# Kernel optimization log

Hardware: AMD Instinct MI355X
Metric: run time of the kernel (lower is better)

Reference implementation:

```python
import math
import jax
import jax.numpy as jnp
from jax import lax
import numpy as np

B, T, S, C, E = 16, 1024, 2048, 256, 256
STRIDE, MAX_SAMPLES, SIGMA, RAND_START = 20, 20, 3.0, 0


def setup_inputs():
    key = jax.random.key(0)
    ks = jax.random.split(key, 6)
    return {
        "x": jax.random.normal(ks[0], (B, T, C), jnp.float32),
        "target_embedding": jax.random.normal(ks[1], (B, T, E), jnp.float32),
        # scale keys so pre-softmax scores are O(1..10) like a trained model
        "enc_keys": jax.random.normal(ks[2], (B, E, S), jnp.float32) * 0.05,
        "enc_values": jax.random.normal(ks[3], (B, S, E), jnp.float32),
        "W_in": jax.random.normal(ks[4], (E, C), jnp.float32) * math.sqrt(1.0 / C),
        "b_in": jnp.zeros((E,), jnp.float32),
        "W_out": jax.random.normal(ks[5], (C, E), jnp.float32) * math.sqrt(1.0 / E),
        "b_out": jnp.zeros((C,), jnp.float32),
    }


def _get_matrix(attn, sim_vec, stride, start):
    # attn: [B,T,S], sim_vec: [B,S,E]
    nrm = sim_vec / jnp.linalg.norm(sim_vec, axis=2, keepdims=True)
    attn_avg = jnp.mean(attn, axis=1)[..., None]          # [B,S,1]
    ns = nrm[:, start::stride, :]                          # [B,N,E]
    aa = attn_avg[:, start::stride, :]                     # [B,N,1]
    sim = jnp.einsum('bne,bme->bnm', ns, ns)               # cosine similarity
    qual = aa @ jnp.swapaxes(aa, 1, 2)                     # quality outer product
    return qual * sim                                      # DPP kernel L [B,N,N]


def _bfgm(L, max_samples):
    # Vectorized faithful version of the greedy Cholesky DPP MAP loop.
    Bv, N, _ = L.shape
    bidx = jnp.arange(Bv)
    D0 = jnp.diagonal(L, axis1=1, axis2=2)                 # [B,N]
    mask0 = jnp.ones((Bv, N), L.dtype)
    J0 = jnp.argmax(jnp.log(D0 * mask0), axis=1)
    mask0 = mask0.at[bidx, J0].set(0.0)
    C0 = jnp.zeros((Bv, N, max_samples), L.dtype)          # col 0 stays zero (as in torch)

    def step(carry, t):
        Cm, D, J, mask = carry
        Lj = L[bidx, J, :]                                 # [B,N] = L[b, J[b], i]
        cj = Cm[bidx, J, :]                                # [B,K]
        cdot = jnp.einsum('bnk,bk->bn', Cm, cj)            # <c_i, c_j>
        dj = D[bidx, J][:, None]
        e = (Lj - cdot) / dj * mask                        # zero at already-selected
        Cm = Cm.at[:, :, t].set(e)
        D = D - e * e
        J = jnp.argmax(jnp.log(D * mask), axis=1)
        mask = mask.at[bidx, J].set(0.0)
        return (Cm, D, J, mask), J

    (_, _, _, _), Js = lax.scan(step, (C0, D0, J0, mask0), jnp.arange(1, max_samples))
    all_J = jnp.concatenate([J0[None, :], Js], axis=0).T   # [B,max_samples]
    return jnp.sort(all_J, axis=1)                         # = nonzero(1-mask) order


def _create_gm(mu, sigma, length):
    pos = jnp.arange(length, dtype=jnp.float32)            # [S]
    z = pos[None, None, :] - mu[:, :, None].astype(jnp.float32)
    g = jnp.exp(-(z * z) / (2.0 * sigma * sigma)) / (math.sqrt(2.0 * math.pi) * sigma)
    return jnp.sum(g, axis=1)                              # [B,S]


def _forward(x, target_embedding, enc_keys, enc_values, W_in, b_in, W_out, b_out):
    residual = x
    h = (jnp.einsum('btc,ec->bte', x, W_in) + b_in + target_embedding) * math.sqrt(0.5)
    scores = jnp.einsum('bte,bes->bts', h, enc_keys)       # [B,T,S]
    attn = jax.nn.softmax(scores, axis=-1)
    # DPP auxiliary KL loss (training path, encoder_padding_mask=None); the
    # kernel / greedy selection / target distribution carry no gradient.
    L = _get_matrix(lax.stop_gradient(attn), lax.stop_gradient(enc_values), STRIDE, RAND_START)
    mu = _bfgm(L, MAX_SAMPLES)
    dist = jax.nn.softmax(_create_gm(mu, SIGMA, scores.shape[2]), axis=1)
    x_mean = jnp.mean(attn, axis=1)                        # [B,S]
    kl = jnp.sum(x_mean * (jnp.log(x_mean) - dist))        # KLDivLoss(input=dist, target=x_mean, sum)
    out = jnp.einsum('bts,bse->bte', attn, enc_values)
    s = enc_values.shape[1]
    out = out * (s * math.sqrt(1.0 / s))                   # = sqrt(s)
    out = (jnp.einsum('bte,ce->btc', out, W_out) + b_out + residual) * math.sqrt(0.5)
    return out, attn, -kl


def reference(x, target_embedding, enc_keys, enc_values, W_in, b_in, W_out, b_out):
    return _forward(x, target_embedding, enc_keys, enc_values, W_in, b_in, W_out, b_out)
```

## Files before the change

### kernel.cpp

```cpp
#include <hip/hip_runtime.h>
#include <math.h>

#define BB 16
#define TT 1024
#define SS 2048
#define CC 256
#define EE 256
#define NSUB 103
#define MAXS 20
#define STRIDE_ 20
#define XCH 32

static constexpr float RSQRT2  = 0.70710678118654752440f;
static constexpr float SQRT_S  = 45.25483399593904f;
static constexpr float GNORM   = 0.13298076013381093f;
static constexpr float INV2S2  = 0.055555555555555555f;

typedef __attribute__((ext_vector_type(8))) __bf16 bf16x8;
typedef __attribute__((ext_vector_type(4))) float  f32x4;

__device__ __forceinline__ float wave_sum(float v) {
    #pragma unroll
    for (int o = 32; o; o >>= 1) v += __shfl_down(v, o);
    return v;
}
__device__ __forceinline__ float wave_max(float v) {
    #pragma unroll
    for (int o = 32; o; o >>= 1) v = fmaxf(v, __shfl_down(v, o));
    return v;
}
__device__ __forceinline__ unsigned short f2bf(float f) {
    unsigned int u = __float_as_uint(f);
    u = (u + 0x7FFFu + ((u >> 16) & 1u)) >> 16;
    return (unsigned short)u;
}
__device__ __forceinline__ float bf2f(unsigned short s) {
    return __uint_as_float(((unsigned int)s) << 16);
}

#define GLD_LDS16(g, l) __builtin_amdgcn_global_load_lds(                      \
    (const __attribute__((address_space(1))) void*)(g),                        \
    (__attribute__((address_space(3))) void*)(l), 16, 0, 0)

__global__ __launch_bounds__(256) void k_cast3(
    const float* __restrict__ a,  unsigned short* __restrict__ oa, int na,
    const float* __restrict__ b2, unsigned short* __restrict__ ob, int nb,
    const float* __restrict__ c2, unsigned short* __restrict__ oc, int nc)
{
    int i = blockIdx.x * 256 + threadIdx.x;
    const float* in; unsigned short* out;
    if (i < na)                { in = a;  out = oa; }
    else if (i < na + nb)      { in = b2; out = ob; i -= na; }
    else if (i < na + nb + nc) { in = c2; out = oc; i -= na + nb; }
    else return;
    const float4 v = reinterpret_cast<const float4*>(in)[i];
    union { unsigned short u[4]; unsigned long long v8; } pk;
    pk.u[0] = f2bf(v.x); pk.u[1] = f2bf(v.y);
    pk.u[2] = f2bf(v.z); pk.u[3] = f2bf(v.w);
    reinterpret_cast<unsigned long long*>(out)[i] = pk.v8;
}

__global__ __launch_bounds__(256) void k_transpose2(
    const float* __restrict__ keys, unsigned short* __restrict__ keysT,
    const float* __restrict__ vals, unsigned short* __restrict__ valsT)
{
    __shared__ float t[64][65];
    const int id = blockIdx.x;
    const float* in; unsigned short* out;
    int R, Cc, bx, by, b;
    if (id < 2048) {
        in = keys; out = keysT; R = EE; Cc = SS;
        bx = id & 3; by = (id >> 2) & 31; b = id >> 7;
    } else {
        const int id2 = id - 2048;
        in = vals; out = valsT; R = SS; Cc = EE;
        bx = id2 & 31; by = (id2 >> 5) & 3; b = id2 >> 7;
    }
    const int r0 = bx * 64, c0 = by * 64;
    const float* ip = in + (size_t)b * R * Cc;
    unsigned short* op = out + (size_t)b * R * Cc;
    const int tx = threadIdx.x & 63, ty = threadIdx.x >> 6;
    #pragma unroll
    for (int i = 0; i < 16; ++i)
        t[ty + 4 * i][tx] = ip[(size_t)(r0 + ty + 4 * i) * Cc + c0 + tx];
    __syncthreads();
    #pragma unroll
    for (int i = 0; i < 16; ++i)
        op[(size_t)(c0 + ty + 4 * i) * R + r0 + tx] = f2bf(t[tx][ty + 4 * i]);
}

template<int BM, int BN, int MODE>
__global__ __launch_bounds__(256) void k_gemm(
    const unsigned short* __restrict__ Abase,
    const unsigned short* __restrict__ Btbase,
    const float* __restrict__ bias, const float* __restrict__ add,
    float* __restrict__ Obase, unsigned short* __restrict__ Obbase,
    int M, int Nn, int K, float scale)
{
    constexpr int BK = 64;
    constexpr int AR = BM / 32;
    constexpr int BR = BN / 32;
    constexpr int WM = BM / 2, WN = BN / 2;
    constexpr int MI = WM / 16, NJ = WN / 16;

    __shared__ unsigned short As[BM * BK];
    __shared__ unsigned short Bs[BN * BK];

    const int nwg = gridDim.x * gridDim.y * gridDim.z;
    int l = blockIdx.x + gridDim.x * (blockIdx.y + gridDim.y * blockIdx.z);
    if ((nwg & 7) == 0) l = (l & 7) * (nwg >> 3) + (l >> 3);
    const int bx = l % gridDim.x; l /= gridDim.x;
    const int by = l % gridDim.y;
    const int b  = l / gridDim.y;

    const int m0 = bx * BM;
    const int n0 = by * BN;
    const unsigned short* A  = Abase  + (size_t)b * M  * K;
    const unsigned short* Bt = Btbase + (size_t)b * Nn * K;

    const int tid  = threadIdx.x;
    const int w    = tid >> 6;
    const int lane = tid & 63;
    const int wm   = w & 1, wn = w >> 1;

    const int sr  = tid >> 3;
    const int skb = ((tid & 7) << 4) ^ ((sr & 7) << 4);
    const unsigned short* ga[AR];
    const unsigned short* gb[BR];
    #pragma unroll
    for (int p = 0; p < AR; ++p)
        ga[p] = A + (size_t)(m0 + p * 32 + sr) * K + (skb >> 1);
    #pragma unroll
    for (int p = 0; p < BR; ++p)
        gb[p] = Bt + (size_t)(n0 + p * 32 + sr) * K + (skb >> 1);

    const int fr = lane & 15;
    const int qb = (lane >> 4) << 4;

    f32x4 acc[MI][NJ];
    #pragma unroll
    for (int i = 0; i < MI; ++i)
        #pragma unroll
        for (int j = 0; j < NJ; ++j)
            acc[i][j] = (f32x4){0.f, 0.f, 0.f, 0.f};

    for (int k0 = 0; k0 < K; k0 += BK) {
        #pragma unroll
        for (int p = 0; p < AR; ++p) GLD_LDS16(ga[p], As + p * 2048 + w * 512);
        #pragma unroll
        for (int p = 0; p < BR; ++p) GLD_LDS16(gb[p], Bs + p * 2048 + w * 512);
        #pragma unroll
        for (int p = 0; p < AR; ++p) ga[p] += BK;
        #pragma unroll
        for (int p = 0; p < BR; ++p) gb[p] += BK;
        __syncthreads();
        #pragma unroll
        for (int c = 0; c < 2; ++c) {
            bf16x8 af[MI], bf[NJ];
            #pragma unroll
            for (int i = 0; i < MI; ++i) {
                const int row = wm * WM + i * 16 + fr;
                const int byt = row * 128 + ((c * 64 + qb) ^ ((row & 7) << 4));
                af[i] = *reinterpret_cast<const bf16x8*>(
                            reinterpret_cast<const char*>(As) + byt);
            }
            #pragma unroll
            for (int j = 0; j < NJ; ++j) {
                const int row = wn * WN + j * 16 + fr;
                const int byt = row * 128 + ((c * 64 + qb) ^ ((row & 7) << 4));
                bf[j] = *reinterpret_cast<const bf16x8*>(
                            reinterpret_cast<const char*>(Bs) + byt);
            }
            #pragma unroll
            for (int i = 0; i < MI; ++i)
                #pragma unroll
                for (int j = 0; j < NJ; ++j)
                    acc[i][j] = __builtin_amdgcn_mfma_f32_16x16x32_bf16(af[i], bf[j], acc[i][j], 0, 0, 0);
        }
        __syncthreads();
    }

    float* Of = (MODE == 0 || MODE == 1) ? Obase + (size_t)b * M * Nn : nullptr;
    unsigned short* Ob = (MODE == 2 || MODE == 3) ? Obbase + (size_t)b * M * Nn : nullptr;
    const int rb = (lane >> 4) * 4;
    #pragma unroll
    for (int i = 0; i < MI; ++i)
        #pragma unroll
        for (int j = 0; j < NJ; ++j) {
            const int n = n0 + wn * WN + j * 16 + fr;
            #pragma unroll
            for (int r2 = 0; r2 < 4; ++r2) {
                const int m = m0 + wm * WM + i * 16 + rb + r2;
                const size_t idx = (size_t)m * Nn + n;
                if (MODE == 0) {
                    Of[idx] = acc[i][j][r2] * scale;
                } else if (MODE == 1) {
                    Of[idx] = (acc[i][j][r2] + bias[n] + add[idx]) * RSQRT2;
                } else if (MODE == 2) {
                    Ob[idx] = f2bf((acc[i][j][r2] + bias[n] + add[idx]) * RSQRT2);
                } else {
                    Ob[idx] = f2bf(acc[i][j][r2] * scale);
                }
            }
        }
}

__global__ __launch_bounds__(256) void k_softmax(float* __restrict__ attn,
                                                 unsigned short* __restrict__ attnb)
{
    const int row  = blockIdx.x * 4 + (threadIdx.x >> 6);
    const int lane = threadIdx.x & 63;
    float* p = attn + (size_t)row * SS;
    unsigned short* pb = attnb + (size_t)row * SS;

    float v[32];
    #pragma unroll
    for (int s = 0; s < 4; ++s) {
        union { unsigned short u[8]; uint4 q; } ld;
        ld.q = *reinterpret_cast<const uint4*>(&pb[s * 512 + lane * 8]);
        #pragma unroll
        for (int i = 0; i < 8; ++i) v[s * 8 + i] = bf2f(ld.u[i]);
    }
    float mx = v[0];
    #pragma unroll
    for (int i = 1; i < 32; ++i) mx = fmaxf(mx, v[i]);
    #pragma unroll
    for (int o = 32; o; o >>= 1) mx = fmaxf(mx, __shfl_xor(mx, o));
    float s = 0.f;
    #pragma unroll
    for (int i = 0; i < 32; ++i) { v[i] = expf(v[i] - mx); s += v[i]; }
    #pragma unroll
    for (int o = 32; o; o >>= 1) s += __shfl_xor(s, o);
    const float inv = 1.0f / s;
    #pragma unroll
    for (int seg = 0; seg < 4; ++seg) {
        float4 o0, o1;
        o0.x = v[seg * 8 + 0] * inv; o0.y = v[seg * 8 + 1] * inv;
        o0.z = v[seg * 8 + 2] * inv; o0.w = v[seg * 8 + 3] * inv;
        o1.x = v[seg * 8 + 4] * inv; o1.y = v[seg * 8 + 5] * inv;
        o1.z = v[seg * 8 + 6] * inv; o1.w = v[seg * 8 + 7] * inv;
        *reinterpret_cast<float4*>(&p[seg * 512 + lane * 8])     = o0;
        *reinterpret_cast<float4*>(&p[seg * 512 + lane * 8 + 4]) = o1;
        union { unsigned short u[8]; uint4 q; } pk;
        pk.u[0] = f2bf(o0.x); pk.u[1] = f2bf(o0.y); pk.u[2] = f2bf(o0.z); pk.u[3] = f2bf(o0.w);
        pk.u[4] = f2bf(o1.x); pk.u[5] = f2bf(o1.y); pk.u[6] = f2bf(o1.z); pk.u[7] = f2bf(o1.w);
        *reinterpret_cast<uint4*>(&pb[seg * 512 + lane * 8]) = pk.q;
    }
}

__global__ __launch_bounds__(256) void k_xmean_part(const unsigned short* __restrict__ attnb,
                                                    float* __restrict__ part,
                                                    float* __restrict__ klp)
{
    const int c = blockIdx.x, b = blockIdx.y;
    if (c == 0 && b == 0 && threadIdx.x == 0) klp[0] = 0.0f;
    const unsigned short* p = attnb + ((size_t)b * TT + (size_t)c * (TT / XCH)) * SS
                              + threadIdx.x * 8;
    float acc[8] = {0.f, 0.f, 0.f, 0.f, 0.f, 0.f, 0.f, 0.f};
    #pragma unroll 8
    for (int t = 0; t < TT / XCH; ++t) {
        union { unsigned short u[8]; uint4 v4; } ld;
        ld.v4 = *reinterpret_cast<const uint4*>(p + (size_t)t * SS);
        #pragma unroll
        for (int i = 0; i < 8; ++i) acc[i] += bf2f(ld.u[i]);
    }
    float* o = part + ((size_t)b * XCH + c) * SS + threadIdx.x * 8;
    #pragma unroll
    for (int i = 0; i < 8; ++i) o[i] = acc[i];
}

__global__ __launch_bounds__(128) void k_L_direct(const float* __restrict__ ev,
                                                  const float* __restrict__ part,
                                                  float* __restrict__ Lm)
{
    const int i = blockIdx.x, b = blockIdx.y;
    const int tid = threadIdx.x;
    __shared__ float evi[EE];
    __shared__ float aaS[NSUB];
    __shared__ float w[2];
    const float* rowi = ev + ((size_t)b * SS + (size_t)i * STRIDE_) * EE;
    const float v0 = rowi[tid], v1 = rowi[tid + 128];
    evi[tid] = v0; evi[tid + 128] = v1;
    const float r = wave_sum(v0 * v0 + v1 * v1);
    if ((tid & 63) == 0) w[tid >> 6] = r;
    if (tid < NSUB) {
        float s = 0.f;
        #pragma unroll 8
        for (int c2 = 0; c2 < XCH; ++c2)
            s += part[((size_t)b * XCH + c2) * SS + tid * STRIDE_];
        aaS[tid] = s * (1.0f / TT);
    }
    __syncthreads();
    const float nrmi = sqrtf(w[0] + w[1]);
    const float ai = aaS[i];
    for (int j = tid; j < NSUB; j += 128) {
        const float* rj = ev + ((size_t)b * SS + (size_t)j * STRIDE_) * EE;
        float d = 0.f, n2 = 0.f;
        #pragma unroll 4
        for (int e = 0; e < EE; e += 4) {
            const float4 a4 = *reinterpret_cast<const float4*>(&evi[e]);
            const float4 b4 = *reinterpret_cast<const float4*>(&rj[e]);
            d  += a4.x * b4.x + a4.y * b4.y + a4.z * b4.z + a4.w * b4.w;
            n2 += b4.x * b4.x + b4.y * b4.y + b4.z * b4.z + b4.w * b4.w;
        }
        Lm[((size_t)b * NSUB + i) * NSUB + j] = d * ai * aaS[j] / (nrmi * sqrtf(n2));
    }
}

__global__ __launch_bounds__(256) void k_bfgm_kl(const float* __restrict__ Lm,
                                                 const float* __restrict__ part,
                                                 float* __restrict__ outkl)
{
    const int b = blockIdx.x;
    const int tid = threadIdx.x;
    const float* L = Lm + (size_t)b * NSUB * NSUB;
    __shared__ float CmL[128 * 21];
    __shared__ float musS[MAXS];
    __shared__ float w[4];

    float xm[8];
    #pragma unroll
    for (int i = 0; i < 8; ++i) {
        float s = 0.f;
        #pragma unroll 8
        for (int c2 = 0; c2 < XCH; ++c2)
            s += part[((size_t)b * XCH + c2) * SS + tid + (i << 8)];
        xm[i] = s * (1.0f / TT);
    }

    if (tid < 64) {
        const int i0 = tid, i1 = tid + 64;
        const bool a1 = (i1 < NSUB);
        float D0 = L[(size_t)i0 * NSUB + i0];
        float D1 = a1 ? L[(size_t)i1 * NSUB + i1] : 0.0f;
        float m0 = 1.0f, m1 = a1 ? 1.0f : 0.0f;
        #pragma unroll
        for (int k = 0; k < MAXS; ++k) { CmL[i0 * 21 + k] = 0.0f; CmL[i1 * 21 + k] = 0.0f; }
        #pragma unroll 1
        for (int t = 0; t < MAXS; ++t) {
            float k0 = logf(D0 * m0); if (isnan(k0)) k0 = INFINITY;
            float k1 = a1 ? logf(D1 * m1) : -INFINITY; if (isnan(k1)) k1 = INFINITY;
            float v = k0; int idx = i0;
            if (k1 > v) { v = k1; idx = i1; }
            #pragma unroll
            for (int o = 32; o; o >>= 1) {
                const float ov = __shfl_down(v, o);
                const int   oi = __shfl_down(idx, o);
                if (ov > v || (ov == v && oi < idx)) { v = ov; idx = oi; }
            }
            const int J = __shfl(idx, 0);
            if (J == i0) m0 = 0.0f;
            if (J == i1) m1 = 0.0f;
            if (tid == 0) musS[t] = (float)J;
            if (t == MAXS - 1) break;
            const float Dsel = (J >= 64) ? D1 : D0;
            const float dj = __shfl(Dsel, J & 63);
            const float Lj0 = L[(size_t)J * NSUB + i0];
            const float Lj1 = a1 ? L[(size_t)J * NSUB + i1] : 0.0f;
            float cd0 = 0.0f, cd1 = 0.0f;
            for (int k = 1; k <= t; ++k) {
                const float cjk = CmL[J * 21 + k];
                cd0 += CmL[i0 * 21 + k] * cjk;
                cd1 += CmL[i1 * 21 + k] * cjk;
            }
            const float e0 = (Lj0 - cd0) / dj * m0;
            const float e1 = a1 ? (Lj1 - cd1) / dj * m1 : 0.0f;
            CmL[i0 * 21 + t + 1] = e0;
            CmL[i1 * 21 + t + 1] = e1;
            __threadfence_block();
            D0 -= e0 * e0;
            D1 -= e1 * e1;
        }
    }
    __syncthreads();

    float g[8];
    float mx = -INFINITY;
    #pragma unroll
    for (int i = 0; i < 8; ++i) {
        const float s = (float)(tid + (i << 8));
        float acc = 0.f;
        #pragma unroll
        for (int m = 0; m < MAXS; ++m) { const float z = s - musS[m]; acc += expf(-(z * z) * INV2S2); }
        g[i] = acc * GNORM;
        mx = fmaxf(mx, g[i]);
    }
    float wm = wave_max(mx);
    if ((tid & 63) == 0) w[tid >> 6] = wm;
    __syncthreads();
    const float m = fmaxf(fmaxf(w[0], w[1]), fmaxf(w[2], w[3]));
    float sum = 0.f;
    #pragma unroll
    for (int i = 0; i < 8; ++i) { g[i] = expf(g[i] - m); sum += g[i]; }
    __syncthreads();
    float wsv = wave_sum(sum);
    if ((tid & 63) == 0) w[tid >> 6] = wsv;
    __syncthreads();
    const float inv = 1.0f / (w[0] + w[1] + w[2] + w[3]);
    float acc2 = 0.f;
    #pragma unroll
    for (int i = 0; i < 8; ++i)
        acc2 += xm[i] * (logf(xm[i]) - g[i] * inv);
    __syncthreads();
    float wp = wave_sum(acc2);
    if ((tid & 63) == 0) w[tid >> 6] = wp;
    __syncthreads();
    if (tid == 0) atomicAdd(outkl, -(w[0] + w[1] + w[2] + w[3]));
}

extern "C" void kernel_launch(void* const* d_in, const int* in_sizes, int n_in,
                              void* d_out, int out_size, void* d_ws, size_t ws_size,
                              hipStream_t stream)
{
    const float* x     = (const float*)d_in[0];
    const float* te    = (const float*)d_in[1];
    const float* keys  = (const float*)d_in[2];
    const float* vals  = (const float*)d_in[3];
    const float* W_in  = (const float*)d_in[4];
    const float* b_in  = (const float*)d_in[5];
    const float* W_out = (const float*)d_in[6];
    const float* b_out = (const float*)d_in[7];

    float* outp = (float*)d_out;
    float* attn = outp + (size_t)BB * TT * CC;
    float* klp  = attn + (size_t)BB * TT * SS;

    unsigned short* X       = (unsigned short*)d_ws;
    unsigned short* x_bf    = X;
    unsigned short* Win_bf  = x_bf   + (size_t)BB * TT * CC;
    unsigned short* Wout_bf = Win_bf + (size_t)EE * CC;
    unsigned short* h_bf    = Wout_bf+ (size_t)CC * EE;
    unsigned short* keysT   = h_bf   + (size_t)BB * TT * EE;
    unsigned short* valsT   = keysT  + (size_t)BB * SS * EE;
    unsigned short* attnb   = valsT  + (size_t)BB * EE * SS;
    unsigned short* mid_bf  = attnb  + (size_t)BB * TT * SS;
    float* fws   = (float*)(mid_bf + (size_t)BB * TT * EE + 8);
    float* part  = fws;
    float* Lm    = part  + (size_t)BB * XCH * SS;

    {
        const int na = BB * TT * CC / 4, nb = EE * CC / 4, nc = CC * EE / 4;
        const int blocks = (na + nb + nc + 255) / 256;
        k_cast3<<<blocks, 256, 0, stream>>>(x, x_bf, na, W_in, Win_bf, nb, W_out, Wout_bf, nc);
    }
    k_gemm<64, 64, 2><<<dim3(256, 4, 1), 256, 0, stream>>>(
        x_bf, Win_bf, b_in, te, nullptr, h_bf, BB * TT, CC, CC, 1.0f);
    k_transpose2<<<4096, 256, 0, stream>>>(keys, keysT, vals, valsT);
    k_gemm<128, 128, 3><<<dim3(8, 16, BB), 256, 0, stream>>>(
        h_bf, keysT, nullptr, nullptr, nullptr, attnb, TT, SS, EE, 1.0f);
    k_softmax<<<BB * TT / 4, 256, 0, stream>>>(attn, attnb);
    k_xmean_part<<<dim3(XCH, BB), 256, 0, stream>>>(attnb, part, klp);
    k_L_direct<<<dim3(NSUB, BB), 128, 0, stream>>>(vals, part, Lm);
    k_bfgm_kl<<<BB, 256, 0, stream>>>(Lm, part, klp);
    k_gemm<64, 128, 3><<<dim3(16, 2, BB), 256, 0, stream>>>(
        attnb, valsT, nullptr, nullptr, nullptr, mid_bf, TT, EE, SS, SQRT_S);
    k_gemm<64, 64, 1><<<dim3(256, 4, 1), 256, 0, stream>>>(
        mid_bf, Wout_bf, b_out, x, outp, nullptr, BB * TT, CC, CC, 1.0f);
}
```

Before: 443.1 us.

## Fuse softmax with column-mean partials, merge cast and transpose kernels

The softmax kernel now also accumulates per-block column sums of the normalized attention into shared memory and writes the x-mean partials, so the separate pass that re-read the bf16 attention matrix is gone. The cast and transpose kernels are merged into one launch to save a launch. The attn@V GEMM tile shrinks from 64 to 32 rows, doubling its grid to fill more compute units. In exchange, the fused softmax runs only 512 blocks of 512 threads, each handling 32 rows in sequence, which lowers parallelism for this memory-bound pass and adds a shared-memory reduction with several barriers.

Result: slower. 464.9 us (+4.9%).

```diff
diff --git a/kernel.cpp b/kernel.cpp
--- a/kernel.cpp
+++ b/kernel.cpp
@@ -42,30 +42,29 @@
     (const __attribute__((address_space(1))) void*)(g),                        \
     (__attribute__((address_space(3))) void*)(l), 16, 0, 0)
 
-__global__ __launch_bounds__(256) void k_cast3(
+__global__ __launch_bounds__(256) void k_prep(
+    const float* __restrict__ keys, unsigned short* __restrict__ keysT,
+    const float* __restrict__ vals, unsigned short* __restrict__ valsT,
     const float* __restrict__ a,  unsigned short* __restrict__ oa, int na,
     const float* __restrict__ b2, unsigned short* __restrict__ ob, int nb,
     const float* __restrict__ c2, unsigned short* __restrict__ oc, int nc)
 {
-    int i = blockIdx.x * 256 + threadIdx.x;
-    const float* in; unsigned short* out;
-    if (i < na)                { in = a;  out = oa; }
-    else if (i < na + nb)      { in = b2; out = ob; i -= na; }
-    else if (i < na + nb + nc) { in = c2; out = oc; i -= na + nb; }
-    else return;
-    const float4 v = reinterpret_cast<const float4*>(in)[i];
-    union { unsigned short u[4]; unsigned long long v8; } pk;
-    pk.u[0] = f2bf(v.x); pk.u[1] = f2bf(v.y);
-    pk.u[2] = f2bf(v.z); pk.u[3] = f2bf(v.w);
-    reinterpret_cast<unsigned long long*>(out)[i] = pk.v8;
-}
-
-__global__ __launch_bounds__(256) void k_transpose2(
-    const float* __restrict__ keys, unsigned short* __restrict__ keysT,
-    const float* __restrict__ vals, unsigned short* __restrict__ valsT)
-{
+    const int id = blockIdx.x;
+    if (id >= 4096) {
+        int i = (id - 4096) * 256 + threadIdx.x;
+        const float* in; unsigned short* out;
+        if (i < na)                { in = a;  out = oa; }
+        else if (i < na + nb)      { in = b2; out = ob; i -= na; }
+        else if (i < na + nb + nc) { in = c2; out = oc; i -= na + nb; }
+        else return;
+        const float4 v = reinterpret_cast<const float4*>(in)[i];
+        union { unsigned short u[4]; unsigned long long v8; } pk;
+        pk.u[0] = f2bf(v.x); pk.u[1] = f2bf(v.y);
+        pk.u[2] = f2bf(v.z); pk.u[3] = f2bf(v.w);
+        reinterpret_cast<unsigned long long*>(out)[i] = pk.v8;
+        return;
+    }
     __shared__ float t[64][65];
-    const int id = blockIdx.x;
     const float* in; unsigned short* out;
     int R, Cc, bx, by, b;
     if (id < 2048) {
@@ -205,68 +204,74 @@
         }
 }
 
-__global__ __launch_bounds__(256) void k_softmax(float* __restrict__ attn,
-                                                 unsigned short* __restrict__ attnb)
-{
-    const int row  = blockIdx.x * 4 + (threadIdx.x >> 6);
-    const int lane = threadIdx.x & 63;
-    float* p = attn + (size_t)row * SS;
-    unsigned short* pb = attnb + (size_t)row * SS;
-
-    float v[32];
-    #pragma unroll
-    for (int s = 0; s < 4; ++s) {
-        union { unsigned short u[8]; uint4 q; } ld;
-        ld.q = *reinterpret_cast<const uint4*>(&pb[s * 512 + lane * 8]);
-        #pragma unroll
-        for (int i = 0; i < 8; ++i) v[s * 8 + i] = bf2f(ld.u[i]);
-    }
-    float mx = v[0];
-    #pragma unroll
-    for (int i = 1; i < 32; ++i) mx = fmaxf(mx, v[i]);
-    #pragma unroll
-    for (int o = 32; o; o >>= 1) mx = fmaxf(mx, __shfl_xor(mx, o));
-    float s = 0.f;
-    #pragma unroll
-    for (int i = 0; i < 32; ++i) { v[i] = expf(v[i] - mx); s += v[i]; }
-    #pragma unroll
-    for (int o = 32; o; o >>= 1) s += __shfl_xor(s, o);
-    const float inv = 1.0f / s;
-    #pragma unroll
-    for (int seg = 0; seg < 4; ++seg) {
-        float4 o0, o1;
-        o0.x = v[seg * 8 + 0] * inv; o0.y = v[seg * 8 + 1] * inv;
-        o0.z = v[seg * 8 + 2] * inv; o0.w = v[seg * 8 + 3] * inv;
-        o1.x = v[seg * 8 + 4] * inv; o1.y = v[seg * 8 + 5] * inv;
-        o1.z = v[seg * 8 + 6] * inv; o1.w = v[seg * 8 + 7] * inv;
-        *reinterpret_cast<float4*>(&p[seg * 512 + lane * 8])     = o0;
-        *reinterpret_cast<float4*>(&p[seg * 512 + lane * 8 + 4]) = o1;
-        union { unsigned short u[8]; uint4 q; } pk;
-        pk.u[0] = f2bf(o0.x); pk.u[1] = f2bf(o0.y); pk.u[2] = f2bf(o0.z); pk.u[3] = f2bf(o0.w);
-        pk.u[4] = f2bf(o1.x); pk.u[5] = f2bf(o1.y); pk.u[6] = f2bf(o1.z); pk.u[7] = f2bf(o1.w);
-        *reinterpret_cast<uint4*>(&pb[seg * 512 + lane * 8]) = pk.q;
-    }
-}
-
-__global__ __launch_bounds__(256) void k_xmean_part(const unsigned short* __restrict__ attnb,
-                                                    float* __restrict__ part,
-                                                    float* __restrict__ klp)
+__global__ __launch_bounds__(512) void k_softmax_xmean(
+    float* __restrict__ attn, unsigned short* __restrict__ attnb,
+    float* __restrict__ part, float* __restrict__ klp)
 {
     const int c = blockIdx.x, b = blockIdx.y;
-    if (c == 0 && b == 0 && threadIdx.x == 0) klp[0] = 0.0f;
-    const unsigned short* p = attnb + ((size_t)b * TT + (size_t)c * (TT / XCH)) * SS
-                              + threadIdx.x * 8;
-    float acc[8] = {0.f, 0.f, 0.f, 0.f, 0.f, 0.f, 0.f, 0.f};
-    #pragma unroll 8
-    for (int t = 0; t < TT / XCH; ++t) {
-        union { unsigned short u[8]; uint4 v4; } ld;
-        ld.v4 = *reinterpret_cast<const uint4*>(p + (size_t)t * SS);
-        #pragma unroll
-        for (int i = 0; i < 8; ++i) acc[i] += bf2f(ld.u[i]);
-    }
-    float* o = part + ((size_t)b * XCH + c) * SS + threadIdx.x * 8;
-    #pragma unroll
-    for (int i = 0; i < 8; ++i) o[i] = acc[i];
+    const int tid = threadIdx.x;
+    if (c == 0 && b == 0 && tid == 0) klp[0] = 0.0f;
+    const int wv = tid >> 6, lane = tid & 63;
+    __shared__ float colsum[2][2048];
+    for (int i = tid; i < 2048; i += 512) { colsum[0][i] = 0.f; colsum[1][i] = 0.f; }
+
+    float colacc[32];
+    #pragma unroll
+    for (int i = 0; i < 32; ++i) colacc[i] = 0.f;
+
+    const size_t row0 = (size_t)b * TT + (size_t)c * 32 + wv * 4;
+    for (int r = 0; r < 4; ++r) {
+        float* p = attn + (row0 + r) * SS;
+        unsigned short* pb = attnb + (row0 + r) * SS;
+        float v[32];
+        #pragma unroll
+        for (int sg = 0; sg < 4; ++sg) {
+            union { unsigned short u[8]; uint4 q; } ld;
+            ld.q = *reinterpret_cast<const uint4*>(&pb[sg * 512 + lane * 8]);
+            #pragma unroll
+            for (int i = 0; i < 8; ++i) v[sg * 8 + i] = bf2f(ld.u[i]);
+        }
+        float mx = v[0];
+        #pragma unroll
+        for (int i = 1; i < 32; ++i) mx = fmaxf(mx, v[i]);
+        #pragma unroll
+        for (int o = 32; o; o >>= 1) mx = fmaxf(mx, __shfl_xor(mx, o));
+        float sum = 0.f;
+        #pragma unroll
+        for (int i = 0; i < 32; ++i) { v[i] = expf(v[i] - mx); sum += v[i]; }
+        #pragma unroll
+        for (int o = 32; o; o >>= 1) sum += __shfl_xor(sum, o);
+        const float inv = 1.0f / sum;
+        #pragma unroll
+        for (int sg = 0; sg < 4; ++sg) {
+            float4 o0, o1;
+            o0.x = v[sg * 8 + 0] * inv; o0.y = v[sg * 8 + 1] * inv;
+            o0.z = v[sg * 8 + 2] * inv; o0.w = v[sg * 8 + 3] * inv;
+            o1.x = v[sg * 8 + 4] * inv; o1.y = v[sg * 8 + 5] * inv;
+            o1.z = v[sg * 8 + 6] * inv; o1.w = v[sg * 8 + 7] * inv;
+            *reinterpret_cast<float4*>(&p[sg * 512 + lane * 8])     = o0;
+            *reinterpret_cast<float4*>(&p[sg * 512 + lane * 8 + 4]) = o1;
+            union { unsigned short u[8]; uint4 q; } pk;
+            pk.u[0] = f2bf(o0.x); pk.u[1] = f2bf(o0.y); pk.u[2] = f2bf(o0.z); pk.u[3] = f2bf(o0.w);
+            pk.u[4] = f2bf(o1.x); pk.u[5] = f2bf(o1.y); pk.u[6] = f2bf(o1.z); pk.u[7] = f2bf(o1.w);
+            *reinterpret_cast<uint4*>(&pb[sg * 512 + lane * 8]) = pk.q;
+            colacc[sg * 8 + 0] += o0.x; colacc[sg * 8 + 1] += o0.y;
+            colacc[sg * 8 + 2] += o0.z; colacc[sg * 8 + 3] += o0.w;
+            colacc[sg * 8 + 4] += o1.x; colacc[sg * 8 + 5] += o1.y;
+            colacc[sg * 8 + 6] += o1.z; colacc[sg * 8 + 7] += o1.w;
+        }
+    }
+    __syncthreads();
+    #pragma unroll
+    for (int ph = 0; ph < 4; ++ph) {
+        const int sg = (ph + wv) & 3;
+        float* cs = &colsum[wv >> 2][sg * 512 + lane * 8];
+        #pragma unroll
+        for (int i = 0; i < 8; ++i) cs[i] += colacc[sg * 8 + i];
+        __syncthreads();
+    }
+    float* o = part + ((size_t)b * XCH + c) * SS;
+    for (int i = tid; i < 2048; i += 512) o[i] = colsum[0][i] + colsum[1][i];
 }
 
 __global__ __launch_bounds__(128) void k_L_direct(const float* __restrict__ ev,
@@ -440,19 +445,18 @@
 
     {
         const int na = BB * TT * CC / 4, nb = EE * CC / 4, nc = CC * EE / 4;
-        const int blocks = (na + nb + nc + 255) / 256;
-        k_cast3<<<blocks, 256, 0, stream>>>(x, x_bf, na, W_in, Win_bf, nb, W_out, Wout_bf, nc);
+        const int blocks = 4096 + (na + nb + nc + 255) / 256;
+        k_prep<<<blocks, 256, 0, stream>>>(keys, keysT, vals, valsT,
+                                           x, x_bf, na, W_in, Win_bf, nb, W_out, Wout_bf, nc);
     }
     k_gemm<64, 64, 2><<<dim3(256, 4, 1), 256, 0, stream>>>(
         x_bf, Win_bf, b_in, te, nullptr, h_bf, BB * TT, CC, CC, 1.0f);
-    k_transpose2<<<4096, 256, 0, stream>>>(keys, keysT, vals, valsT);
     k_gemm<128, 128, 3><<<dim3(8, 16, BB), 256, 0, stream>>>(
         h_bf, keysT, nullptr, nullptr, nullptr, attnb, TT, SS, EE, 1.0f);
-    k_softmax<<<BB * TT / 4, 256, 0, stream>>>(attn, attnb);
-    k_xmean_part<<<dim3(XCH, BB), 256, 0, stream>>>(attnb, part, klp);
+    k_softmax_xmean<<<dim3(XCH, BB), 512, 0, stream>>>(attn, attnb, part, klp);
     k_L_direct<<<dim3(NSUB, BB), 128, 0, stream>>>(vals, part, Lm);
     k_bfgm_kl<<<BB, 256, 0, stream>>>(Lm, part, klp);
-    k_gemm<64, 128, 3><<<dim3(16, 2, BB), 256, 0, stream>>>(
+    k_gemm<32, 128, 3><<<dim3(32, 2, BB), 256, 0, stream>>>(
         attnb, valsT, nullptr, nullptr, nullptr, mid_bf, TT, EE, SS, SQRT_S);
     k_gemm<64, 64, 1><<<dim3(256, 4, 1), 256, 0, stream>>>(
         mid_bf, Wout_bf, b_out, x, outp, nullptr, BB * TT, CC, CC, 1.0f);
```
